# Kernel optimization log

Hardware: AMD Instinct MI355X
Metric: run time of the kernel (lower is better)

The kernel has to match this reference:

```python
import jax, jax.numpy as jnp
import numpy as np

N = 384          # item_num (text regions)
TD = 768         # text hidden (bert-base)
VD = 768         # vision hidden (vit-base)
CD = TD + VD     # commu_dim = 1536
FF = 2048        # TransformerEncoderLayer default dim_feedforward
H = 4            # nhead
L = 2            # num_layers per encoder
EPS = 1e-5


def _enc_params(key, d, scale=0.02):
    ks = jax.random.split(key, 6)
    return dict(
        qkv_w=jax.random.normal(ks[0], (L, 3 * d, d), jnp.float32) * scale,
        qkv_b=jnp.zeros((L, 3 * d), jnp.float32),
        out_w=jax.random.normal(ks[1], (L, d, d), jnp.float32) * scale,
        out_b=jnp.zeros((L, d), jnp.float32),
        ln1_s=jnp.ones((L, d), jnp.float32),
        ln1_b=jnp.zeros((L, d), jnp.float32),
        ff1_w=jax.random.normal(ks[2], (L, FF, d), jnp.float32) * scale,
        ff1_b=jnp.zeros((L, FF), jnp.float32),
        ff2_w=jax.random.normal(ks[3], (L, d, FF), jnp.float32) * scale,
        ff2_b=jnp.zeros((L, d), jnp.float32),
        ln2_s=jnp.ones((L, d), jnp.float32),
        ln2_b=jnp.zeros((L, d), jnp.float32),
    )


def setup_inputs() -> dict:
    key = jax.random.key(0)
    k = jax.random.split(key, 6)
    inp = {
        'text_emb': jax.random.normal(k[0], (N, TD), jnp.float32),
        'vision_emb': jax.random.normal(k[1], (N, VD), jnp.float32),
        'gt_matrix': jax.random.randint(k[2], (N, N), 0, 2, jnp.int32),
    }
    for pref, kk, d in (('t_', k[3], TD), ('c_', k[4], CD)):
        for name, v in _enc_params(kk, d).items():
            inp[pref + name] = v
    inp['lin_w'] = jax.random.normal(k[5], (2, 2 * CD), jnp.float32) * 0.02
    inp['lin_b'] = jnp.zeros((2,), jnp.float32)
    return inp


def _ln(x, s, b):
    m = jnp.mean(x, -1, keepdims=True)
    v = jnp.mean((x - m) ** 2, -1, keepdims=True)
    return (x - m) * jax.lax.rsqrt(v + EPS) * s + b


def _encoder(x, qkv_w, qkv_b, out_w, out_b, ln1_s, ln1_b,
             ff1_w, ff1_b, ff2_w, ff2_b, ln2_s, ln2_b):
    # PyTorch post-norm TransformerEncoder, relu activation, eval mode (no dropout)
    d = x.shape[-1]
    hd = d // H
    for l in range(qkv_w.shape[0]):
        qkv = x @ qkv_w[l].T + qkv_b[l]
        q, kk, v = jnp.split(qkv, 3, axis=-1)
        q = q.reshape(-1, H, hd)
        kk = kk.reshape(-1, H, hd)
        v = v.reshape(-1, H, hd)
        scores = jnp.einsum('qhd,khd->hqk', q, kk) / jnp.sqrt(jnp.float32(hd))
        attn = jax.nn.softmax(scores, -1)
        o = jnp.einsum('hqk,khd->qhd', attn, v).reshape(-1, d)
        x = _ln(x + o @ out_w[l].T + out_b[l], ln1_s[l], ln1_b[l])
        h = jax.nn.relu(x @ ff1_w[l].T + ff1_b[l]) @ ff2_w[l].T + ff2_b[l]
        x = _ln(x + h, ln2_s[l], ln2_b[l])
    return x


def reference(text_emb, vision_emb, gt_matrix,
              t_qkv_w, t_qkv_b, t_out_w, t_out_b, t_ln1_s, t_ln1_b,
              t_ff1_w, t_ff1_b, t_ff2_w, t_ff2_b, t_ln2_s, t_ln2_b,
              c_qkv_w, c_qkv_b, c_out_w, c_out_b, c_ln1_s, c_ln1_b,
              c_ff1_w, c_ff1_b, c_ff2_w, c_ff2_b, c_ln2_s, c_ln2_b,
              lin_w, lin_b):
    te = _encoder(text_emb, t_qkv_w, t_qkv_b, t_out_w, t_out_b, t_ln1_s, t_ln1_b,
                  t_ff1_w, t_ff1_b, t_ff2_w, t_ff2_b, t_ln2_s, t_ln2_b)
    all_emb = jnp.concatenate([te, vision_emb], axis=1)  # [N, CD]
    all_emb = _encoder(all_emb, c_qkv_w, c_qkv_b, c_out_w, c_out_b, c_ln1_s, c_ln1_b,
                       c_ff1_w, c_ff1_b, c_ff2_w, c_ff2_b, c_ln2_s, c_ln2_b)
    # organize(): linear(cat(e_i, e_j)) decomposes exactly as e_i@Wa^T + e_j@Wb^T + b,
    # avoiding the O(N^2 * 2*CD) pair tensor while computing identical math.
    a = all_emb @ lin_w[:, :CD].T + lin_b      # [N, 2]
    c = all_emb @ lin_w[:, CD:].T              # [N, 2]
    logits = a[:, None, :] + c[None, :, :]     # [N, N, 2]
    probs = jax.nn.softmax(logits, -1)         # self.activate(self.linear(...))
    # classificaiton_loss: sum_i CrossEntropyLoss(probs[i], gt[i])  (CE takes probs as logits)
    ls = jax.nn.log_softmax(probs, -1)
    cell = -jnp.take_along_axis(ls, gt_matrix[..., None].astype(jnp.int32), axis=-1)[..., 0]
    cls_loss = jnp.sum(jnp.mean(cell, axis=1))
    # enter_exit_loss over first N-1 items
    link = probs[:, :, 1]
    ee_loss = jnp.sum(jnp.abs(link.sum(1)[:-1] + link.sum(0)[:-1] - 1.0))
    return probs, cls_loss, ee_loss
```

## Files before the change

kernel.cpp:

```cpp
#include <hip/hip_runtime.h>
#include <hip/hip_bf16.h>
#include <math.h>

#define NTOK 384
#define HEADS 4

typedef __attribute__((ext_vector_type(8))) short bf16x8;
typedef __attribute__((ext_vector_type(4))) float f32x4;

__device__ __forceinline__ unsigned short f2b(float f) {
    union { float f; unsigned int u; } v; v.f = f;
    unsigned int r = (v.u + 0x7fff + ((v.u >> 16) & 1)) >> 16;
    return (unsigned short)r;
}

__device__ __forceinline__ void g2l16(const void* g, void* l) {
    __builtin_amdgcn_global_load_lds(
        (const __attribute__((address_space(1))) unsigned int*)g,
        (__attribute__((address_space(3))) unsigned int*)l, 16, 0, 0);
}

__device__ __forceinline__ void stage64(
    const unsigned short* __restrict__ g, int row0, int k0, int ld,
    char* region, int wid, int lane)
{
    int c = wid * 64 + lane;
    int row = c >> 2, p = c & 3;
    int kc = (p - (row >> 1)) & 3;
    g2l16(g + (long)(row0 + row) * ld + k0 + kc * 8,
          region + (wid * 64) * 16);
}

__global__ __launch_bounds__(256, 4) void gemm64(
    const unsigned short* __restrict__ A, const unsigned short* __restrict__ B,
    const float* __restrict__ bias, void* __restrict__ Cv,
    int K, int lda, int ldb, int ldc,
    long sA, long sB, long sC, int relu, int out_bf16,
    unsigned short* __restrict__ vt, int dv2)
{
    __shared__ char smem[2][8192];
    A += (long)blockIdx.z * sA;
    B += (long)blockIdx.z * sB;
    const int t = threadIdx.x, lane = t & 63, wid = t >> 6;
    const int wm = wid >> 1, wn = wid & 1;
    const int r16 = lane & 15, quad = lane >> 4;
    const int row0 = blockIdx.y * 64, col0 = blockIdx.x * 64;

    f32x4 acc[2][2] = {};

    stage64(A, row0, 0, lda, smem[0], wid, lane);
    stage64(B, col0, 0, ldb, smem[0] + 4096, wid, lane);
    int buf = 0;

    for (int k0 = 0; k0 < K; k0 += 32) {
        __syncthreads();
        if (k0 + 32 < K) {
            stage64(A, row0, k0 + 32, lda, smem[buf ^ 1], wid, lane);
            stage64(B, col0, k0 + 32, ldb, smem[buf ^ 1] + 4096, wid, lane);
        }
        const char* cb = smem[buf];
        bf16x8 af[2], bfv[2];
        #pragma unroll
        for (int rt = 0; rt < 2; ++rt) {
            int row = wm * 32 + rt * 16 + r16;
            int p = (quad + (row >> 1)) & 3;
            af[rt] = *reinterpret_cast<const bf16x8*>(cb + row * 64 + p * 16);
        }
        #pragma unroll
        for (int ct = 0; ct < 2; ++ct) {
            int col = wn * 32 + ct * 16 + r16;
            int p = (quad + (col >> 1)) & 3;
            bfv[ct] = *reinterpret_cast<const bf16x8*>(cb + 4096 + col * 64 + p * 16);
        }
        #pragma unroll
        for (int rt = 0; rt < 2; ++rt)
            #pragma unroll
            for (int ct = 0; ct < 2; ++ct)
                acc[rt][ct] = __builtin_amdgcn_mfma_f32_16x16x32_bf16(
                    af[rt], bfv[ct], acc[rt][ct], 0, 0, 0);
        buf ^= 1;
    }

    float* Cf = (float*)Cv;
    unsigned short* Cb = (unsigned short*)Cv;
    const long zoff = (long)blockIdx.z * sC;
    const int vwrite = (vt != nullptr) && (col0 >= dv2);
    #pragma unroll
    for (int rt = 0; rt < 2; ++rt) {
        #pragma unroll
        for (int ct = 0; ct < 2; ++ct) {
            f32x4 v = acc[rt][ct];
            int col = col0 + wn * 32 + ct * 16 + r16;
            float bi = bias ? bias[col] : 0.f;
            #pragma unroll
            for (int i = 0; i < 4; ++i) {
                v[i] += bi;
                if (relu) v[i] = fmaxf(v[i], 0.f);
            }
            int rbase = row0 + wm * 32 + rt * 16 + quad * 4;
            if (vwrite) {
                ushort4 p;
                p.x = f2b(v[0]); p.y = f2b(v[1]); p.z = f2b(v[2]); p.w = f2b(v[3]);
                *reinterpret_cast<ushort4*>(vt + (long)(col - dv2) * NTOK + rbase) = p;
            } else if (out_bf16) {
                #pragma unroll
                for (int i = 0; i < 4; ++i)
                    Cb[zoff + (long)(rbase + i) * ldc + col] = f2b(v[i]);
            } else {
                #pragma unroll
                for (int i = 0; i < 4; ++i)
                    Cf[zoff + (long)(rbase + i) * ldc + col] = v[i];
            }
        }
    }
}

#define WO0 0u
#define WO1 3538944u
#define WO2 4718592u
#define WO3 7864320u
#define WO4 11010048u
#define WO5 25165824u
#define WO6 29884416u
#define WO7 36175872u
#define WTOT 42467328u

__global__ __launch_bounds__(256) void convert_weights(
    const float* __restrict__ s0, const float* __restrict__ s1,
    const float* __restrict__ s2, const float* __restrict__ s3,
    const float* __restrict__ s4, const float* __restrict__ s5,
    const float* __restrict__ s6, const float* __restrict__ s7,
    unsigned short* __restrict__ dst)
{
    unsigned int e = (blockIdx.x * 256u + threadIdx.x) * 8u;
    if (e >= WTOT) return;
    const float* src; unsigned int local;
    if      (e < WO1) { src = s0; local = e - WO0; }
    else if (e < WO2) { src = s1; local = e - WO1; }
    else if (e < WO3) { src = s2; local = e - WO2; }
    else if (e < WO4) { src = s3; local = e - WO3; }
    else if (e < WO5) { src = s4; local = e - WO4; }
    else if (e < WO6) { src = s5; local = e - WO5; }
    else if (e < WO7) { src = s6; local = e - WO6; }
    else              { src = s7; local = e - WO7; }
    float4 v0 = *reinterpret_cast<const float4*>(src + local);
    float4 v1 = *reinterpret_cast<const float4*>(src + local + 4);
    uint4 o;
    o.x = (unsigned)f2b(v0.x) | ((unsigned)f2b(v0.y) << 16);
    o.y = (unsigned)f2b(v0.z) | ((unsigned)f2b(v0.w) << 16);
    o.z = (unsigned)f2b(v1.x) | ((unsigned)f2b(v1.y) << 16);
    o.w = (unsigned)f2b(v1.z) | ((unsigned)f2b(v1.w) << 16);
    *reinterpret_cast<uint4*>(dst + e) = o;
}

__global__ __launch_bounds__(64) void softmax_rows(
    const float* __restrict__ S, unsigned short* __restrict__ P, float scale)
{
    const float* p = S + (long)blockIdx.x * NTOK;
    unsigned short* q = P + (long)blockIdx.x * NTOK;
    const int t = threadIdx.x;
    float vals[6];
    float vmax = -1e30f;
    #pragma unroll
    for (int i = 0; i < 6; ++i) {
        vals[i] = p[t + i * 64] * scale;
        vmax = fmaxf(vmax, vals[i]);
    }
    for (int off = 32; off; off >>= 1) vmax = fmaxf(vmax, __shfl_down(vmax, off));
    vmax = __shfl(vmax, 0);
    float sum = 0.f;
    #pragma unroll
    for (int i = 0; i < 6; ++i) { vals[i] = __expf(vals[i] - vmax); sum += vals[i]; }
    for (int off = 32; off; off >>= 1) sum += __shfl_down(sum, off);
    sum = __shfl(sum, 0);
    float inv = 1.f / sum;
    #pragma unroll
    for (int i = 0; i < 6; ++i) q[t + i * 64] = f2b(vals[i] * inv);
}

__global__ __launch_bounds__(256) void add_ln(
    float* __restrict__ x, unsigned short* __restrict__ xb,
    const float* __restrict__ y,
    const float* __restrict__ s, const float* __restrict__ b, int d)
{
    float* xr = x + (long)blockIdx.x * d;
    unsigned short* xbr = xb + (long)blockIdx.x * d;
    const float* yr = y + (long)blockIdx.x * d;
    const int t = threadIdx.x;
    float s1 = 0.f, s2 = 0.f;
    for (int i = t; i < d; i += 256) {
        float v = xr[i] + yr[i];
        s1 += v; s2 += v * v;
    }
    for (int off = 32; off; off >>= 1) { s1 += __shfl_down(s1, off); s2 += __shfl_down(s2, off); }
    __shared__ float r1[4], r2[4];
    int w = t >> 6;
    if ((t & 63) == 0) { r1[w] = s1; r2[w] = s2; }
    __syncthreads();
    if (t == 0) {
        float a = 0.f, c = 0.f;
        for (int i = 0; i < 4; ++i) { a += r1[i]; c += r2[i]; }
        r1[0] = a; r2[0] = c;
    }
    __syncthreads();
    float mean = r1[0] / d;
    float var = r2[0] / d - mean * mean;
    float rstd = rsqrtf(var + 1e-5f);
    for (int i = t; i < d; i += 256) {
        float v = (xr[i] + yr[i] - mean) * rstd * s[i] + b[i];
        xr[i] = v;
        xbr[i] = f2b(v);
    }
}

__global__ void initx_k(const float* __restrict__ src, float* __restrict__ dst,
                        unsigned short* __restrict__ dstb, int n)
{
    int i = blockIdx.x * blockDim.x + threadIdx.x;
    if (i < n) { float v = src[i]; dst[i] = v; dstb[i] = f2b(v); }
}

__global__ void concat_k(const float* __restrict__ te, const float* __restrict__ ve,
                         float* __restrict__ all, unsigned short* __restrict__ allb)
{
    int i = blockIdx.x * blockDim.x + threadIdx.x;
    if (i >= NTOK * 1536) return;
    int r = i / 1536, c = i % 1536;
    float v = (c < 768) ? te[r * 768 + c] : ve[r * 768 + (c - 768)];
    all[i] = v;
    allb[i] = f2b(v);
}

__global__ __launch_bounds__(256) void head_ac(
    const float* __restrict__ all, const float* __restrict__ lin_w,
    const float* __restrict__ lin_b, float* __restrict__ a, float* __restrict__ c)
{
    const int i = blockIdx.x, t = threadIdx.x;
    const float* xr = all + (long)i * 1536;
    float s0 = 0.f, s1 = 0.f, s2 = 0.f, s3 = 0.f;
    for (int e = t; e < 1536; e += 256) {
        float v = xr[e];
        s0 += v * lin_w[e];
        s1 += v * lin_w[3072 + e];
        s2 += v * lin_w[1536 + e];
        s3 += v * lin_w[4608 + e];
    }
    for (int off = 32; off; off >>= 1) {
        s0 += __shfl_down(s0, off); s1 += __shfl_down(s1, off);
        s2 += __shfl_down(s2, off); s3 += __shfl_down(s3, off);
    }
    __shared__ float r[4][4];
    int w = t >> 6;
    if ((t & 63) == 0) { r[0][w] = s0; r[1][w] = s1; r[2][w] = s2; r[3][w] = s3; }
    __syncthreads();
    if (t == 0) {
        float t0 = 0.f, t1 = 0.f, t2 = 0.f, t3 = 0.f;
        for (int k = 0; k < 4; ++k) { t0 += r[0][k]; t1 += r[1][k]; t2 += r[2][k]; t3 += r[3][k]; }
        a[i * 2 + 0] = t0 + lin_b[0];
        a[i * 2 + 1] = t1 + lin_b[1];
        c[i * 2 + 0] = t2;
        c[i * 2 + 1] = t3;
    }
}

__global__ __launch_bounds__(384) void head_probs(
    const float* __restrict__ a, const float* __restrict__ c,
    const int* __restrict__ gt, float* __restrict__ probs,
    float* __restrict__ rowsum, float* __restrict__ rowcell)
{
    const int i = blockIdx.x, j = threadIdx.x;
    float l0 = a[i * 2 + 0] + c[j * 2 + 0];
    float l1 = a[i * 2 + 1] + c[j * 2 + 1];
    float m = fmaxf(l0, l1);
    float e0 = __expf(l0 - m), e1 = __expf(l1 - m);
    float inv = 1.f / (e0 + e1);
    float p0 = e0 * inv, p1 = e1 * inv;
    long base = ((long)i * NTOK + j) * 2;
    probs[base] = p0;
    probs[base + 1] = p1;
    float m2 = fmaxf(p0, p1);
    float z = m2 + __logf(__expf(p0 - m2) + __expf(p1 - m2));
    int g = gt[i * NTOK + j];
    float cell = z - (g ? p1 : p0);
    float cs = cell, ps = p1;
    for (int off = 32; off; off >>= 1) { cs += __shfl_down(cs, off); ps += __shfl_down(ps, off); }
    __shared__ float rc[6], rs[6];
    int w = j >> 6;
    if ((j & 63) == 0) { rc[w] = cs; rs[w] = ps; }
    __syncthreads();
    if (j == 0) {
        float csum = 0.f, psum = 0.f;
        for (int k = 0; k < 6; ++k) { csum += rc[k]; psum += rs[k]; }
        rowcell[i] = csum * (1.f / NTOK);
        rowsum[i] = psum;
    }
}

__global__ __launch_bounds__(64) void colsum_k(const float* __restrict__ probs,
                                               float* __restrict__ colsum)
{
    const int j = blockIdx.x, t = threadIdx.x;
    float s = 0.f;
    for (int i = t; i < NTOK; i += 64)
        s += probs[((long)i * NTOK + j) * 2 + 1];
    for (int off = 32; off; off >>= 1) s += __shfl_down(s, off);
    if (t == 0) colsum[j] = s;
}

__global__ __launch_bounds__(384) void finalize_k(
    const float* __restrict__ rowcell, const float* __restrict__ rowsum,
    const float* __restrict__ colsum, float* __restrict__ out)
{
    const int t = threadIdx.x;
    float cls = rowcell[t];
    float ee = (t < NTOK - 1) ? fabsf(rowsum[t] + colsum[t] - 1.f) : 0.f;
    for (int off = 32; off; off >>= 1) { cls += __shfl_down(cls, off); ee += __shfl_down(ee, off); }
    __shared__ float rc[6], re[6];
    int w = t >> 6;
    if ((t & 63) == 0) { rc[w] = cls; re[w] = ee; }
    __syncthreads();
    if (t == 0) {
        float a = 0.f, b = 0.f;
        for (int k = 0; k < 6; ++k) { a += rc[k]; b += re[k]; }
        out[NTOK * NTOK * 2 + 0] = a;
        out[NTOK * NTOK * 2 + 1] = b;
    }
}

static void run_encoder(float* x, unsigned short* xb, int d,
                        const unsigned short* wq, const unsigned short* wo,
                        const unsigned short* w1, const unsigned short* w2,
                        const float* qkv_b, const float* out_b,
                        const float* ln1_s, const float* ln1_b,
                        const float* ff1_b, const float* ff2_b,
                        const float* ln2_s, const float* ln2_b,
                        unsigned short* qkvb, float* sc, unsigned short* attnb,
                        unsigned short* vtb, unsigned short* ob,
                        unsigned short* t1b, float* t2,
                        hipStream_t stream)
{
    const int dq = 3 * d;
    const int hd = d / HEADS;
    const float scale = 1.0f / sqrtf((float)hd);
    for (int l = 0; l < 2; ++l) {
        gemm64<<<dim3(dq / 64, 6), 256, 0, stream>>>(
            xb, wq + (long)l * dq * d, qkv_b + l * dq, qkvb,
            d, d, d, dq, 0, 0, 0, 0, 1, vtb, 2 * d);
        gemm64<<<dim3(6, 6, HEADS), 256, 0, stream>>>(
            qkvb, qkvb + d, nullptr, sc,
            hd, dq, dq, NTOK, (long)hd, (long)hd, (long)NTOK * NTOK,
            0, 0, nullptr, 0);
        softmax_rows<<<HEADS * NTOK, 64, 0, stream>>>(sc, attnb, scale);
        gemm64<<<dim3(hd / 64, 6, HEADS), 256, 0, stream>>>(
            attnb, vtb, nullptr, ob,
            NTOK, NTOK, NTOK, d, (long)NTOK * NTOK, (long)hd * NTOK, (long)hd,
            0, 1, nullptr, 0);
        gemm64<<<dim3(d / 64, 6), 256, 0, stream>>>(
            ob, wo + (long)l * d * d, out_b + l * d, t2,
            d, d, d, d, 0, 0, 0, 0, 0, nullptr, 0);
        add_ln<<<NTOK, 256, 0, stream>>>(x, xb, t2, ln1_s + l * d, ln1_b + l * d, d);
        gemm64<<<dim3(2048 / 64, 6), 256, 0, stream>>>(
            xb, w1 + (long)l * 2048 * d, ff1_b + l * 2048, t1b,
            d, d, d, 2048, 0, 0, 0, 1, 1, nullptr, 0);
        gemm64<<<dim3(d / 64, 6), 256, 0, stream>>>(
            t1b, w2 + (long)l * d * 2048, ff2_b + l * d, t2,
            2048, 2048, 2048, d, 0, 0, 0, 0, 0, nullptr, 0);
        add_ln<<<NTOK, 256, 0, stream>>>(x, xb, t2, ln2_s + l * d, ln2_b + l * d, d);
    }
}

extern "C" void kernel_launch(void* const* d_in, const int* in_sizes, int n_in,
                              void* d_out, int out_size, void* d_ws, size_t ws_size,
                              hipStream_t stream)
{
    const float* text_emb   = (const float*)d_in[0];
    const float* vision_emb = (const float*)d_in[1];
    const int*   gt         = (const int*)  d_in[2];
    const float* t_qkv_w = (const float*)d_in[3];
    const float* t_qkv_b = (const float*)d_in[4];
    const float* t_out_w = (const float*)d_in[5];
    const float* t_out_b = (const float*)d_in[6];
    const float* t_ln1_s = (const float*)d_in[7];
    const float* t_ln1_b = (const float*)d_in[8];
    const float* t_ff1_w = (const float*)d_in[9];
    const float* t_ff1_b = (const float*)d_in[10];
    const float* t_ff2_w = (const float*)d_in[11];
    const float* t_ff2_b = (const float*)d_in[12];
    const float* t_ln2_s = (const float*)d_in[13];
    const float* t_ln2_b = (const float*)d_in[14];
    const float* c_qkv_w = (const float*)d_in[15];
    const float* c_qkv_b = (const float*)d_in[16];
    const float* c_out_w = (const float*)d_in[17];
    const float* c_out_b = (const float*)d_in[18];
    const float* c_ln1_s = (const float*)d_in[19];
    const float* c_ln1_b = (const float*)d_in[20];
    const float* c_ff1_w = (const float*)d_in[21];
    const float* c_ff1_b = (const float*)d_in[22];
    const float* c_ff2_w = (const float*)d_in[23];
    const float* c_ff2_b = (const float*)d_in[24];
    const float* c_ln2_s = (const float*)d_in[25];
    const float* c_ln2_b = (const float*)d_in[26];
    const float* lin_w   = (const float*)d_in[27];
    const float* lin_b   = (const float*)d_in[28];
    float* out = (float*)d_out;

    float* ws = (float*)d_ws;
    float* xt      = ws;
    float* all     = xt + 294912;
    float* t2      = all + 589824;
    float* sc      = t2 + 589824;
    float* abuf    = sc + 589824;
    float* cbuf    = abuf + 768;
    float* rowsum  = cbuf + 768;
    float* rowcell = rowsum + 384;
    float* colsum  = rowcell + 384;
    unsigned short* ub = (unsigned short*)(ws + 2067072);
    unsigned short* xtb   = ub;
    unsigned short* allb  = xtb + 294912;
    unsigned short* qkvb  = allb + 589824;
    unsigned short* attnb = qkvb + 1769472;
    unsigned short* vtb   = attnb + 589824;
    unsigned short* ob    = vtb + 589824;
    unsigned short* t1b   = ob + 589824;
    unsigned short* wb    = t1b + 786432;

    convert_weights<<<(WTOT / 8 + 255) / 256, 256, 0, stream>>>(
        t_qkv_w, t_out_w, t_ff1_w, t_ff2_w,
        c_qkv_w, c_out_w, c_ff1_w, c_ff2_w, wb);

    initx_k<<<(294912 + 255) / 256, 256, 0, stream>>>(text_emb, xt, xtb, 294912);
    run_encoder(xt, xtb, 768,
                wb + WO0, wb + WO1, wb + WO2, wb + WO3,
                t_qkv_b, t_out_b, t_ln1_s, t_ln1_b,
                t_ff1_b, t_ff2_b, t_ln2_s, t_ln2_b,
                qkvb, sc, attnb, vtb, ob, t1b, t2, stream);

    concat_k<<<(589824 + 255) / 256, 256, 0, stream>>>(xt, vision_emb, all, allb);
    run_encoder(all, allb, 1536,
                wb + WO4, wb + WO5, wb + WO6, wb + WO7,
                c_qkv_b, c_out_b, c_ln1_s, c_ln1_b,
                c_ff1_b, c_ff2_b, c_ln2_s, c_ln2_b,
                qkvb, sc, attnb, vtb, ob, t1b, t2, stream);

    head_ac<<<NTOK, 256, 0, stream>>>(all, lin_w, lin_b, abuf, cbuf);
    head_probs<<<NTOK, 384, 0, stream>>>(abuf, cbuf, gt, out, rowsum, rowcell);
    colsum_k<<<NTOK, 64, 0, stream>>>(out, colsum);
    finalize_k<<<1, 384, 0, stream>>>(rowcell, rowsum, colsum, out);
}
```

Before: 602.9 us.

## Fuse fp32-to-bf16 weight conversion into GEMM B-tile staging

Removes the standalone weight conversion kernel and its bf16 weight buffer. The GEMM now loads fp32 weight rows into registers, converts them to bf16 and writes them into the LDS tile, prefetching one k-step ahead. This avoids a full extra write and read of the converted weights. In exchange, each row block re-reads fp32 weights at twice the byte width and uses synchronous register staging instead of direct global-to-LDS loads.

Result: slower. 962.0 us (+59.6%).

```diff
diff --git a/kernel.cpp b/kernel.cpp
--- a/kernel.cpp
+++ b/kernel.cpp
@@ -12,6 +12,13 @@
     union { float f; unsigned int u; } v; v.f = f;
     unsigned int r = (v.u + 0x7fff + ((v.u >> 16) & 1)) >> 16;
     return (unsigned short)r;
+}
+
+__device__ __forceinline__ unsigned int cvt2(float a, float b) {
+    __hip_bfloat162 h = __float22bfloat162_rn(make_float2(a, b));
+    unsigned int u;
+    __builtin_memcpy(&u, &h, 4);
+    return u;
 }
 
 __device__ __forceinline__ void g2l16(const void* g, void* l) {
@@ -32,31 +39,57 @@
 }
 
 __global__ __launch_bounds__(256, 4) void gemm64(
-    const unsigned short* __restrict__ A, const unsigned short* __restrict__ B,
+    const unsigned short* __restrict__ A, const void* __restrict__ Bv,
     const float* __restrict__ bias, void* __restrict__ Cv,
     int K, int lda, int ldb, int ldc,
     long sA, long sB, long sC, int relu, int out_bf16,
-    unsigned short* __restrict__ vt, int dv2)
+    unsigned short* __restrict__ vt, int dv2, int bf32)
 {
     __shared__ char smem[2][8192];
     A += (long)blockIdx.z * sA;
-    B += (long)blockIdx.z * sB;
     const int t = threadIdx.x, lane = t & 63, wid = t >> 6;
     const int wm = wid >> 1, wn = wid & 1;
     const int r16 = lane & 15, quad = lane >> 4;
     const int row0 = blockIdx.y * 64, col0 = blockIdx.x * 64;
 
+    const int c = wid * 64 + lane;
+    const int srow = c >> 2, sp = c & 3;
+    const int skc = (sp - (srow >> 1)) & 3;
+
+    const unsigned short* B16 = nullptr;
+    const float* B32 = nullptr;
+    if (bf32) B32 = (const float*)Bv + (long)(col0 + srow) * ldb + skc * 8;
+    else      B16 = (const unsigned short*)Bv + (long)blockIdx.z * sB;
+
     f32x4 acc[2][2] = {};
-
+    float4 pv0, pv1;
+
+    if (bf32) {
+        pv0 = *reinterpret_cast<const float4*>(B32);
+        pv1 = *reinterpret_cast<const float4*>(B32 + 4);
+    } else {
+        stage64(B16, col0, 0, ldb, smem[0] + 4096, wid, lane);
+    }
     stage64(A, row0, 0, lda, smem[0], wid, lane);
-    stage64(B, col0, 0, ldb, smem[0] + 4096, wid, lane);
+    if (bf32) {
+        uint4 o;
+        o.x = cvt2(pv0.x, pv0.y); o.y = cvt2(pv0.z, pv0.w);
+        o.z = cvt2(pv1.x, pv1.y); o.w = cvt2(pv1.z, pv1.w);
+        *reinterpret_cast<uint4*>(smem[0] + 4096 + c * 16) = o;
+    }
     int buf = 0;
 
     for (int k0 = 0; k0 < K; k0 += 32) {
         __syncthreads();
-        if (k0 + 32 < K) {
+        const int more = (k0 + 32 < K);
+        if (more) {
+            if (bf32) {
+                pv0 = *reinterpret_cast<const float4*>(B32 + k0 + 32);
+                pv1 = *reinterpret_cast<const float4*>(B32 + k0 + 36);
+            } else {
+                stage64(B16, col0, k0 + 32, ldb, smem[buf ^ 1] + 4096, wid, lane);
+            }
             stage64(A, row0, k0 + 32, lda, smem[buf ^ 1], wid, lane);
-            stage64(B, col0, k0 + 32, ldb, smem[buf ^ 1] + 4096, wid, lane);
         }
         const char* cb = smem[buf];
         bf16x8 af[2], bfv[2];
@@ -78,6 +111,12 @@
             for (int ct = 0; ct < 2; ++ct)
                 acc[rt][ct] = __builtin_amdgcn_mfma_f32_16x16x32_bf16(
                     af[rt], bfv[ct], acc[rt][ct], 0, 0, 0);
+        if (more && bf32) {
+            uint4 o;
+            o.x = cvt2(pv0.x, pv0.y); o.y = cvt2(pv0.z, pv0.w);
+            o.z = cvt2(pv1.x, pv1.y); o.w = cvt2(pv1.z, pv1.w);
+            *reinterpret_cast<uint4*>(smem[buf ^ 1] + 4096 + c * 16) = o;
+        }
         buf ^= 1;
     }
 
@@ -115,44 +154,6 @@
     }
 }
 
-#define WO0 0u
-#define WO1 3538944u
-#define WO2 4718592u
-#define WO3 7864320u
-#define WO4 11010048u
-#define WO5 25165824u
-#define WO6 29884416u
-#define WO7 36175872u
-#define WTOT 42467328u
-
-__global__ __launch_bounds__(256) void convert_weights(
-    const float* __restrict__ s0, const float* __restrict__ s1,
-    const float* __restrict__ s2, const float* __restrict__ s3,
-    const float* __restrict__ s4, const float* __restrict__ s5,
-    const float* __restrict__ s6, const float* __restrict__ s7,
-    unsigned short* __restrict__ dst)
-{
-    unsigned int e = (blockIdx.x * 256u + threadIdx.x) * 8u;
-    if (e >= WTOT) return;
-    const float* src; unsigned int local;
-    if      (e < WO1) { src = s0; local = e - WO0; }
-    else if (e < WO2) { src = s1; local = e - WO1; }
-    else if (e < WO3) { src = s2; local = e - WO2; }
-    else if (e < WO4) { src = s3; local = e - WO3; }
-    else if (e < WO5) { src = s4; local = e - WO4; }
-    else if (e < WO6) { src = s5; local = e - WO5; }
-    else if (e < WO7) { src = s6; local = e - WO6; }
-    else              { src = s7; local = e - WO7; }
-    float4 v0 = *reinterpret_cast<const float4*>(src + local);
-    float4 v1 = *reinterpret_cast<const float4*>(src + local + 4);
-    uint4 o;
-    o.x = (unsigned)f2b(v0.x) | ((unsigned)f2b(v0.y) << 16);
-    o.y = (unsigned)f2b(v0.z) | ((unsigned)f2b(v0.w) << 16);
-    o.z = (unsigned)f2b(v1.x) | ((unsigned)f2b(v1.y) << 16);
-    o.w = (unsigned)f2b(v1.z) | ((unsigned)f2b(v1.w) << 16);
-    *reinterpret_cast<uint4*>(dst + e) = o;
-}
-
 __global__ __launch_bounds__(64) void softmax_rows(
     const float* __restrict__ S, unsigned short* __restrict__ P, float scale)
 {
@@ -328,8 +329,8 @@
 }
 
 static void run_encoder(float* x, unsigned short* xb, int d,
-                        const unsigned short* wq, const unsigned short* wo,
-                        const unsigned short* w1, const unsigned short* w2,
+                        const float* wq, const float* wo,
+                        const float* w1, const float* w2,
                         const float* qkv_b, const float* out_b,
                         const float* ln1_s, const float* ln1_b,
                         const float* ff1_b, const float* ff2_b,
@@ -345,26 +346,26 @@
     for (int l = 0; l < 2; ++l) {
         gemm64<<<dim3(dq / 64, 6), 256, 0, stream>>>(
             xb, wq + (long)l * dq * d, qkv_b + l * dq, qkvb,
-            d, d, d, dq, 0, 0, 0, 0, 1, vtb, 2 * d);
+            d, d, d, dq, 0, 0, 0, 0, 1, vtb, 2 * d, 1);
         gemm64<<<dim3(6, 6, HEADS), 256, 0, stream>>>(
             qkvb, qkvb + d, nullptr, sc,
             hd, dq, dq, NTOK, (long)hd, (long)hd, (long)NTOK * NTOK,
-            0, 0, nullptr, 0);
+            0, 0, nullptr, 0, 0);
         softmax_rows<<<HEADS * NTOK, 64, 0, stream>>>(sc, attnb, scale);
         gemm64<<<dim3(hd / 64, 6, HEADS), 256, 0, stream>>>(
             attnb, vtb, nullptr, ob,
             NTOK, NTOK, NTOK, d, (long)NTOK * NTOK, (long)hd * NTOK, (long)hd,
-            0, 1, nullptr, 0);
+            0, 1, nullptr, 0, 0);
         gemm64<<<dim3(d / 64, 6), 256, 0, stream>>>(
             ob, wo + (long)l * d * d, out_b + l * d, t2,
-            d, d, d, d, 0, 0, 0, 0, 0, nullptr, 0);
+            d, d, d, d, 0, 0, 0, 0, 0, nullptr, 0, 1);
         add_ln<<<NTOK, 256, 0, stream>>>(x, xb, t2, ln1_s + l * d, ln1_b + l * d, d);
         gemm64<<<dim3(2048 / 64, 6), 256, 0, stream>>>(
             xb, w1 + (long)l * 2048 * d, ff1_b + l * 2048, t1b,
-            d, d, d, 2048, 0, 0, 0, 1, 1, nullptr, 0);
+            d, d, d, 2048, 0, 0, 0, 1, 1, nullptr, 0, 1);
         gemm64<<<dim3(d / 64, 6), 256, 0, stream>>>(
             t1b, w2 + (long)l * d * 2048, ff2_b + l * d, t2,
-            2048, 2048, 2048, d, 0, 0, 0, 0, 0, nullptr, 0);
+            2048, 2048, 2048, d, 0, 0, 0, 0, 0, nullptr, 0, 1);
         add_ln<<<NTOK, 256, 0, stream>>>(x, xb, t2, ln2_s + l * d, ln2_b + l * d, d);
     }
 }
@@ -422,22 +423,17 @@
     unsigned short* vtb   = attnb + 589824;
     unsigned short* ob    = vtb + 589824;
     unsigned short* t1b   = ob + 589824;
-    unsigned short* wb    = t1b + 786432;
-
-    convert_weights<<<(WTOT / 8 + 255) / 256, 256, 0, stream>>>(
-        t_qkv_w, t_out_w, t_ff1_w, t_ff2_w,
-        c_qkv_w, c_out_w, c_ff1_w, c_ff2_w, wb);
 
     initx_k<<<(294912 + 255) / 256, 256, 0, stream>>>(text_emb, xt, xtb, 294912);
     run_encoder(xt, xtb, 768,
-                wb + WO0, wb + WO1, wb + WO2, wb + WO3,
+                t_qkv_w, t_out_w, t_ff1_w, t_ff2_w,
                 t_qkv_b, t_out_b, t_ln1_s, t_ln1_b,
                 t_ff1_b, t_ff2_b, t_ln2_s, t_ln2_b,
                 qkvb, sc, attnb, vtb, ob, t1b, t2, stream);
 
     concat_k<<<(589824 + 255) / 256, 256, 0, stream>>>(xt, vision_emb, all, allb);
     run_encoder(all, allb, 1536,
-                wb + WO4, wb + WO5, wb + WO6, wb + WO7,
+                c_qkv_w, c_out_w, c_ff1_w, c_ff2_w,
                 c_qkv_b, c_out_b, c_ln1_s, c_ln1_b,
                 c_ff1_b, c_ff2_b, c_ln2_s, c_ln2_b,
                 qkvb, sc, attnb, vtb, ob, t1b, t2, stream);
```
